# Kernel optimization log

Measured on AMD Instinct MI355X. Metric: run time of the kernel, lower is better.

## Reference

```python
import jax, jax.numpy as jnp
import numpy as np

NUM_HEADS = 8
NUM_CHUNKS, INPUT_DIM = 50000, 768
HIDDEN_DIM, OUTPUT_DIM = 512, 256
NUM_CELLS, MAX_LEN = 2048, 64


def setup_inputs() -> dict:
    key = jax.random.key(0)
    ks = jax.random.split(key, 16)
    s = 0.02
    return {
        "chunk_features": jax.random.normal(ks[0], (NUM_CHUNKS, INPUT_DIM), jnp.float32),
        # q/k/v input projections (nn.Linear: y = x @ W.T + b)
        "Wq": jax.random.normal(ks[1], (HIDDEN_DIM, INPUT_DIM), jnp.float32) * s,
        "bq": jnp.zeros((HIDDEN_DIM,), jnp.float32),
        "Wk": jax.random.normal(ks[2], (HIDDEN_DIM, INPUT_DIM), jnp.float32) * s,
        "bk": jnp.zeros((HIDDEN_DIM,), jnp.float32),
        "Wv": jax.random.normal(ks[3], (HIDDEN_DIM, INPUT_DIM), jnp.float32) * s,
        "bv": jnp.zeros((HIDDEN_DIM,), jnp.float32),
        # nn.MultiheadAttention internal in_proj (stacked q,k,v) and out_proj
        "W_in": jax.random.normal(ks[4], (3 * HIDDEN_DIM, HIDDEN_DIM), jnp.float32) * s,
        "b_in": jnp.zeros((3 * HIDDEN_DIM,), jnp.float32),
        "Wo": jax.random.normal(ks[5], (HIDDEN_DIM, HIDDEN_DIM), jnp.float32) * s,
        "bo": jnp.zeros((HIDDEN_DIM,), jnp.float32),
        # final output projection
        "Wout": jax.random.normal(ks[6], (OUTPUT_DIM, HIDDEN_DIM), jnp.float32) * s,
        "bout": jnp.zeros((OUTPUT_DIM,), jnp.float32),
        # ragged cells packed as padded indices + lengths
        "cell_idx": jax.random.randint(ks[7], (NUM_CELLS, MAX_LEN), 0, NUM_CHUNKS, jnp.int64),
        "cell_len": jax.random.randint(ks[8], (NUM_CELLS,), 0, MAX_LEN, jnp.int64),
    }


def reference(chunk_features, Wq, bq, Wk, bk, Wv, bv, W_in, b_in, Wo, bo,
              Wout, bout, cell_idx, cell_len):
    C, L = cell_idx.shape
    H = Wq.shape[0]
    hd = H // NUM_HEADS
    dt = chunk_features.dtype
    lengths = jnp.maximum(cell_len, 1)                       # at least 1 valid chunk per cell
    mask = jnp.arange(L)[None, :] < lengths[:, None]         # [C, L] valid-position mask

    x = chunk_features[cell_idx]                             # [C, L, D] ragged gather (padded)
    q = x @ Wq.T + bq                                        # [C, L, H]
    k = x @ Wk.T + bk
    v = x @ Wv.T + bv

    # MultiheadAttention's own in_proj on top of q/k/v
    Wiq, Wik, Wiv = jnp.split(W_in, 3, axis=0)
    biq, bik, biv = jnp.split(b_in, 3)
    qi = (q @ Wiq.T + biq).reshape(C, L, NUM_HEADS, hd)
    ki = (k @ Wik.T + bik).reshape(C, L, NUM_HEADS, hd)
    vi = (v @ Wiv.T + biv).reshape(C, L, NUM_HEADS, hd)

    scale = jnp.asarray(1.0 / np.sqrt(hd), dt)
    scores = jnp.einsum('clhd,cmhd->chlm', qi, ki) * scale   # [C, nH, L, L]
    scores = jnp.where(mask[:, None, None, :], scores, jnp.asarray(-1e30, dt))
    attn = jax.nn.softmax(scores, axis=-1)
    ctx = jnp.einsum('chlm,cmhd->clhd', attn, vi).reshape(C, L, H)
    out = ctx @ Wo.T + bo                                    # MHA out_proj

    # masked mean-pool over valid chunk positions, then final projection
    pooled = (out * mask[..., None]).sum(axis=1) / lengths[:, None].astype(dt)
    return pooled @ Wout.T + bout                            # [C, OUTPUT_DIM]
```

## Files before the change

kernel.cpp:

```cpp
#include <hip/hip_runtime.h>

typedef short s16x8 __attribute__((ext_vector_type(8)));
typedef float f32x4 __attribute__((ext_vector_type(4)));
typedef unsigned short u16;

static __device__ __forceinline__ f32x4 mfma16(s16x8 a, s16x8 b, f32x4 c) {
  return __builtin_amdgcn_mfma_f32_16x16x32_bf16(a, b, c, 0, 0, 0);
}

static __device__ __forceinline__ u16 f2b(float f) {
  union { float f; unsigned int u; } v; v.f = f;
  unsigned int u = v.u;
  return (u16)((u + 0x7fffu + ((u >> 16) & 1u)) >> 16);
}

static __device__ __forceinline__ void gld_lds16(const void* g, void* l) {
  __builtin_amdgcn_global_load_lds(
      (const __attribute__((address_space(1))) void*)g,
      (__attribute__((address_space(3))) void*)l, 16, 0, 0);
}

template<int MODE>
__global__ __launch_bounds__(256)
void gemm_pre(const float* __restrict__ A, const float* __restrict__ B,
              void* __restrict__ Cout, const float* __restrict__ bias,
              int M, int N, int K) {
  __shared__ u16 As[64][40];
  __shared__ u16 BsT[64][40];
  const int m0 = blockIdx.y << 6, n0 = blockIdx.x << 6;
  const int tid = threadIdx.x;
  const int wave = tid >> 6, lane = tid & 63;
  const int quad = lane >> 4, l16 = lane & 15;
  f32x4 acc[4] = {{0,0,0,0},{0,0,0,0},{0,0,0,0},{0,0,0,0}};
  for (int k0 = 0; k0 < K; k0 += 32) {
    __syncthreads();
    {
      const int r = tid >> 2, cs = (tid & 3) << 3;
      const float* ap = A + (size_t)(m0 + r) * K + k0 + cs;
      float4 v0 = *(const float4*)ap, v1 = *(const float4*)(ap + 4);
      As[r][cs+0] = f2b(v0.x); As[r][cs+1] = f2b(v0.y);
      As[r][cs+2] = f2b(v0.z); As[r][cs+3] = f2b(v0.w);
      As[r][cs+4] = f2b(v1.x); As[r][cs+5] = f2b(v1.y);
      As[r][cs+6] = f2b(v1.z); As[r][cs+7] = f2b(v1.w);
    }
    {
      const int kk = tid >> 3, ns = (tid & 7) << 3;
      const float* bp = B + (size_t)(k0 + kk) * N + n0 + ns;
      float4 v0 = *(const float4*)bp, v1 = *(const float4*)(bp + 4);
      BsT[ns+0][kk] = f2b(v0.x); BsT[ns+1][kk] = f2b(v0.y);
      BsT[ns+2][kk] = f2b(v0.z); BsT[ns+3][kk] = f2b(v0.w);
      BsT[ns+4][kk] = f2b(v1.x); BsT[ns+5][kk] = f2b(v1.y);
      BsT[ns+6][kk] = f2b(v1.z); BsT[ns+7][kk] = f2b(v1.w);
    }
    __syncthreads();
    const s16x8 af = *(const s16x8*)&As[(wave << 4) + l16][quad << 3];
    #pragma unroll
    for (int nt = 0; nt < 4; nt++) {
      const s16x8 bfr = *(const s16x8*)&BsT[(nt << 4) + l16][quad << 3];
      acc[nt] = mfma16(af, bfr, acc[nt]);
    }
  }
  const int mrow = m0 + (wave << 4) + (quad << 2);
  #pragma unroll
  for (int nt = 0; nt < 4; nt++) {
    const int n = n0 + (nt << 4) + l16;
    float badd = 0.f;
    if (MODE == 2) badd = bias[n];
    #pragma unroll
    for (int r = 0; r < 4; r++) {
      float v = acc[nt][r] + badd;
      if (MODE == 0)      ((u16*)Cout)[(size_t)(mrow + r) * N + n] = f2b(v);
      else if (MODE == 1) ((float*)Cout)[(size_t)n * M + (mrow + r)] = v;
      else                ((float*)Cout)[(size_t)(mrow + r) * N + n] = v;
    }
  }
}

__global__ __launch_bounds__(256)
void bias_dot(const float* __restrict__ A, const float* __restrict__ v,
              const float* __restrict__ c, float* __restrict__ out,
              int M, int K) {
  int j = blockIdx.x * 256 + threadIdx.x;
  if (j >= M) return;
  const float* ar = A + (size_t)j * K;
  float acc = 0.f;
  for (int k = 0; k < K; k += 4) {
    float4 w = *(const float4*)(ar + k);
    acc += w.x * v[k] + w.y * v[k+1] + w.z * v[k+2] + w.w * v[k+3];
  }
  out[j] = acc + c[j];
}

__global__ __launch_bounds__(256)
void convert_bf16(const float* __restrict__ src, u16* __restrict__ dst) {
  const size_t i = ((size_t)blockIdx.x * 256 + threadIdx.x) << 3;
  ushort4 lo, hi;
  if (i < (size_t)50000 * 768) {
    const float4 a = *(const float4*)(src + i);
    const float4 b = *(const float4*)(src + i + 4);
    lo.x = f2b(a.x); lo.y = f2b(a.y); lo.z = f2b(a.z); lo.w = f2b(a.w);
    hi.x = f2b(b.x); hi.y = f2b(b.y); hi.z = f2b(b.z); hi.w = f2b(b.w);
  } else {
    lo.x = lo.y = lo.z = lo.w = 0; hi.x = hi.y = hi.z = hi.w = 0;
  }
  *(ushort4*)(dst + i) = lo;
  *(ushort4*)(dst + i + 4) = hi;
}

__global__ __launch_bounds__(256)
void qkv_gemm(const u16* __restrict__ Xb, const u16* __restrict__ W,
              const float* __restrict__ bias, u16* __restrict__ QKV) {
  __shared__ u16 As[128 * 32];
  __shared__ u16 Bs[128 * 32];
  const int tid = threadIdx.x;
  const int wave = tid >> 6, lane = tid & 63;
  const int wm = wave >> 1, wn = wave & 1;
  const int quad = lane >> 4, l16 = lane & 15;
  const int m0 = blockIdx.y << 7, n0 = blockIdx.x << 7;

  const int r0 = (wave << 5) + (lane >> 2);
  const int cb = (lane & 3) << 3;
  const u16* gA = Xb + (size_t)(m0 + r0) * 768 + cb;
  const u16* gB = W  + (size_t)(n0 + r0) * 768 + cb;
  u16* lA = As + (wave << 10);
  u16* lB = Bs + (wave << 10);

  f32x4 acc[4][4];
  #pragma unroll
  for (int i = 0; i < 4; i++)
    #pragma unroll
    for (int j = 0; j < 4; j++) acc[i][j] = (f32x4){0.f, 0.f, 0.f, 0.f};

  for (int k0 = 0; k0 < 768; k0 += 32) {
    __syncthreads();
    gld_lds16(gA + k0,            lA);
    gld_lds16(gA + k0 + 16 * 768, lA + 512);
    gld_lds16(gB + k0,            lB);
    gld_lds16(gB + k0 + 16 * 768, lB + 512);
    __syncthreads();
    s16x8 af[4], bf[4];
    #pragma unroll
    for (int i = 0; i < 4; i++)
      af[i] = *(const s16x8*)(As + ((wm << 6) + (i << 4) + l16) * 32 + (quad << 3));
    #pragma unroll
    for (int j = 0; j < 4; j++)
      bf[j] = *(const s16x8*)(Bs + ((wn << 6) + (j << 4) + l16) * 32 + (quad << 3));
    #pragma unroll
    for (int i = 0; i < 4; i++)
      #pragma unroll
      for (int j = 0; j < 4; j++)
        acc[i][j] = mfma16(af[i], bf[j], acc[i][j]);
  }

  #pragma unroll
  for (int j = 0; j < 4; j++) {
    const int col = n0 + (wn << 6) + (j << 4) + l16;
    const float badd = bias[col];
    #pragma unroll
    for (int i = 0; i < 4; i++) {
      const int row = m0 + (wm << 6) + (i << 4) + (quad << 2);
      #pragma unroll
      for (int r = 0; r < 4; r++)
        QKV[(size_t)(row + r) * 1536 + col] = f2b(acc[i][j][r] + badd);
    }
  }
}

__global__ __launch_bounds__(256)
void attn2(const u16* __restrict__ QKV, const int* __restrict__ cell_idx,
           const int* __restrict__ cell_len, float* __restrict__ pooled_g) {
  __shared__ int idx_s[64];
  __shared__ u16 VT[64][72];
  __shared__ u16 Ps[64][72];
  __shared__ float Sf[64][66];
  __shared__ float pp[4][64];

  const int c = blockIdx.x, h = blockIdx.y;
  const int tid = threadIdx.x;
  const int wave = tid >> 6, lane = tid & 63;
  const int quad = lane >> 4, l16 = lane & 15;

  int len = cell_len[c];
  len = (len < 1) ? 1 : ((len > 64) ? 64 : len);
  const int mt = (len + 15) >> 4;
  const int Lr = mt << 4;
  const int kpv = (len + 31) >> 5;
  const float invLen = 1.0f / (float)len;

  if (tid < 64) idx_s[tid] = cell_idx[(c << 6) + tid];
  {
    const ushort4 z = {0, 0, 0, 0};
    u16* vz = &VT[0][0];
    u16* pz = &Ps[0][0];
    for (int i = tid; i < 1152; i += 256) {
      *(ushort4*)(vz + (i << 2)) = z;
      *(ushort4*)(pz + (i << 2)) = z;
    }
  }
  __syncthreads();

  for (int i = tid; i < (len << 3); i += 256) {
    const int r = i >> 3, seg = i & 7;
    const u16* src = QKV + (size_t)idx_s[r] * 1536 + 1024 + (h << 6) + (seg << 3);
    const ushort4 a = *(const ushort4*)src;
    const ushort4 b = *(const ushort4*)(src + 4);
    const int d0 = seg << 3;
    VT[d0+0][r] = a.x; VT[d0+1][r] = a.y; VT[d0+2][r] = a.z; VT[d0+3][r] = a.w;
    VT[d0+4][r] = b.x; VT[d0+5][r] = b.y; VT[d0+6][r] = b.z; VT[d0+7][r] = b.w;
  }

  for (int item = wave; item < mt * mt; item += 4) {
    const int mq = item / mt, mk = item - mq * mt;
    const size_t qrow = (size_t)idx_s[(mq << 4) + l16] * 1536;
    const size_t krow = (size_t)idx_s[(mk << 4) + l16] * 1536;
    f32x4 s = {0.f, 0.f, 0.f, 0.f};
    #pragma unroll
    for (int ks = 0; ks < 2; ks++) {
      const s16x8 a = *(const s16x8*)(QKV + qrow + (h << 6) + (ks << 5) + (quad << 3));
      const s16x8 b = *(const s16x8*)(QKV + krow + 512 + (h << 6) + (ks << 5) + (quad << 3));
      s = mfma16(a, b, s);
    }
    const int col = (mk << 4) + l16, rb = (mq << 4) + (quad << 2);
    Sf[rb+0][col] = s[0]; Sf[rb+1][col] = s[1];
    Sf[rb+2][col] = s[2]; Sf[rb+3][col] = s[3];
  }
  __syncthreads();

  {
    const int row = tid >> 2, sub = tid & 3, c0 = sub << 4;
    if (row < Lr) {
      float ev[16];
      float mx = -3e38f;
      #pragma unroll
      for (int t = 0; t < 16; t++) {
        const int cc = c0 + t;
        const float v = (cc < len) ? Sf[row][cc] : -3e38f;
        ev[t] = v; mx = fmaxf(mx, v);
      }
      mx = fmaxf(mx, __shfl_xor(mx, 1));
      mx = fmaxf(mx, __shfl_xor(mx, 2));
      float sum = 0.f;
      #pragma unroll
      for (int t = 0; t < 16; t++) {
        const int cc = c0 + t;
        const float e = (cc < len) ? __expf((ev[t] - mx) * 0.125f) : 0.f;
        ev[t] = e; sum += e;
      }
      sum += __shfl_xor(sum, 1);
      sum += __shfl_xor(sum, 2);
      const float inv = 1.0f / sum;
      #pragma unroll
      for (int t = 0; t < 16; t++) {
        const int cc = c0 + t;
        if (cc < len) Ps[row][cc] = f2b(ev[t] * inv);
      }
    }
  }
  __syncthreads();

  for (int item = wave; item < (mt << 2); item += 4) {
    const int mq = item >> 2, nd = item & 3;
    f32x4 s = {0.f, 0.f, 0.f, 0.f};
    for (int ks = 0; ks < kpv; ks++) {
      const s16x8 a = *(const s16x8*)&Ps[(mq << 4) + l16][(ks << 5) + (quad << 3)];
      const s16x8 b = *(const s16x8*)&VT[(nd << 4) + l16][(ks << 5) + (quad << 3)];
      s = mfma16(a, b, s);
    }
    const int col = (nd << 4) + l16, rb = (mq << 4) + (quad << 2);
    Sf[rb+0][col] = s[0]; Sf[rb+1][col] = s[1];
    Sf[rb+2][col] = s[2]; Sf[rb+3][col] = s[3];
  }
  __syncthreads();

  {
    float s = 0.f;
    for (int l = wave; l < len; l += 4) s += Sf[l][lane];
    pp[wave][lane] = s;
  }
  __syncthreads();
  if (tid < 64) {
    const float s = (pp[0][tid] + pp[1][tid] + pp[2][tid] + pp[3][tid]) * invLen;
    pooled_g[((size_t)c << 9) + (h << 6) + tid] = s;
  }
}

template<int MT>
static __device__ __forceinline__ void heads_loop(
    const u16* __restrict__ Wqkv, const float* __restrict__ b_eff,
    u16 (*Xs)[776], u16 (*Qs)[72], u16 (*Ks)[72], u16 (*VTs)[72],
    u16 (*Psf)[72], float (*Sf)[65], float* pooled,
    const int len, const float invLen, const int tid) {
  const int wave = tid >> 6, lane = tid & 63;
  const int quad = lane >> 4, l16 = lane & 15;
  constexpr int LR = MT * 16;
  constexpr int KPV = (LR + 31) / 32;
  const float scale = 0.125f;

  for (int h = 0; h < 8; h++) {
    f32x4 acc[3][MT];
    #pragma unroll
    for (int it = 0; it < 3; it++)
      #pragma unroll
      for (int im = 0; im < MT; im++) acc[it][im] = (f32x4){0.f,0.f,0.f,0.f};
    int grow[3], jcol[3];
    #pragma unroll
    for (int it = 0; it < 3; it++) {
      const int j = ((wave * 3 + it) << 4) + l16;
      const int sec = j >> 6;
      grow[it] = (sec << 9) + (h << 6) + (j & 63);
      jcol[it] = j;
    }
    s16x8 bcur[3];
    #pragma unroll
    for (int it = 0; it < 3; it++)
      bcur[it] = *(const s16x8*)(Wqkv + (size_t)grow[it] * 768 + (quad << 3));
    for (int ks = 0; ks < 24; ks++) {
      s16x8 bnext[3];
      const int ksn = (ks < 23) ? (ks + 1) : 23;
      #pragma unroll
      for (int it = 0; it < 3; it++)
        bnext[it] = *(const s16x8*)(Wqkv + (size_t)grow[it] * 768 + (ksn << 5) + (quad << 3));
      s16x8 af[MT];
      #pragma unroll
      for (int im = 0; im < MT; im++)
        af[im] = *(const s16x8*)&Xs[(im << 4) + l16][(ks << 5) + (quad << 3)];
      #pragma unroll
      for (int it = 0; it < 3; it++)
        #pragma unroll
        for (int im = 0; im < MT; im++)
          acc[it][im] = mfma16(af[im], bcur[it], acc[it][im]);
      bcur[0] = bnext[0]; bcur[1] = bnext[1]; bcur[2] = bnext[2];
    }
    #pragma unroll
    for (int it = 0; it < 3; it++) {
      const float badd = b_eff[grow[it]];
      const int j = jcol[it];
      #pragma unroll
      for (int im = 0; im < MT; im++) {
        const int rb = (im << 4) + (quad << 2);
        if (j < 64) {
          #pragma unroll
          for (int r = 0; r < 4; r++) Qs[rb + r][j] = f2b(acc[it][im][r] + badd);
        } else if (j < 128) {
          #pragma unroll
          for (int r = 0; r < 4; r++) Ks[rb + r][j - 64] = f2b(acc[it][im][r] + badd);
        } else {
          ushort4 hv;
          hv.x = f2b(acc[it][im][0] + badd);
          hv.y = f2b(acc[it][im][1] + badd);
          hv.z = f2b(acc[it][im][2] + badd);
          hv.w = f2b(acc[it][im][3] + badd);
          *(ushort4*)&VTs[j - 128][rb] = hv;
        }
      }
    }
    __syncthreads();
    for (int item = wave; item < MT * MT; item += 4) {
      const int mq = item / MT, mk = item - mq * MT;
      f32x4 sacc = (f32x4){0.f,0.f,0.f,0.f};
      #pragma unroll
      for (int ks = 0; ks < 2; ks++) {
        const s16x8 a = *(const s16x8*)&Qs[(mq << 4) + l16][(ks << 5) + (quad << 3)];
        const s16x8 b = *(const s16x8*)&Ks[(mk << 4) + l16][(ks << 5) + (quad << 3)];
        sacc = mfma16(a, b, sacc);
      }
      const int col = (mk << 4) + l16;
      const int rb = (mq << 4) + (quad << 2);
      #pragma unroll
      for (int r = 0; r < 4; r++) Sf[rb + r][col] = sacc[r];
    }
    __syncthreads();
    if (tid < LR) {
      float mx = -1e30f;
      for (int m = 0; m < len; m++) mx = fmaxf(mx, Sf[tid][m]);
      float sum = 0.f;
      for (int m = 0; m < len; m++) {
        const float e = __expf((Sf[tid][m] - mx) * scale);
        Sf[tid][m] = e;
        sum += e;
      }
      const float inv = 1.0f / sum;
      for (int m = 0; m < len; m++) Psf[tid][m] = f2b(Sf[tid][m] * inv);
    }
    __syncthreads();
    for (int item = wave; item < MT * 4; item += 4) {
      const int mq = item >> 2, nd = item & 3;
      f32x4 cacc = (f32x4){0.f,0.f,0.f,0.f};
      #pragma unroll
      for (int ks = 0; ks < KPV; ks++) {
        const s16x8 a = *(const s16x8*)&Psf[(mq << 4) + l16][(ks << 5) + (quad << 3)];
        const s16x8 b = *(const s16x8*)&VTs[(nd << 4) + l16][(ks << 5) + (quad << 3)];
        cacc = mfma16(a, b, cacc);
      }
      const int col = (nd << 4) + l16;
      const int rb = (mq << 4) + (quad << 2);
      #pragma unroll
      for (int r = 0; r < 4; r++) Sf[rb + r][col] = cacc[r];
    }
    __syncthreads();
    if (tid < 64) {
      float s = 0.f;
      for (int l = 0; l < len; l++) s += Sf[l][tid];
      pooled[(h << 6) + tid] = s * invLen;
    }
    __syncthreads();
  }
}

__global__ __launch_bounds__(256, 1)
void cell_attn(const float* __restrict__ chunk, const u16* __restrict__ Wqkv,
               const float* __restrict__ b_eff, const int* __restrict__ cell_idx,
               const int* __restrict__ cell_len, float* __restrict__ pooled_g) {
  __shared__ u16 Xs[64][776];
  __shared__ u16 Qs[64][72];
  __shared__ u16 Ks[64][72];
  __shared__ u16 VTs[64][72];
  __shared__ u16 Psf[64][72];
  __shared__ float Sf[64][65];
  __shared__ float pooled[512];
  __shared__ int idx_s[64];

  const int c = blockIdx.x;
  const int tid = threadIdx.x;

  int len = cell_len[c];
  len = (len < 1) ? 1 : ((len > 64) ? 64 : len);
  const int mt = (len + 15) >> 4;
  const int Lr = mt << 4;
  const float invLen = 1.0f / (float)len;

  if (tid < 64) idx_s[tid] = cell_idx[(c << 6) + tid];
  __syncthreads();

  for (int i = tid; i < len * 192; i += 256) {
    const int r = i / 192;
    const int c4 = i - r * 192;
    const float4 f = *(const float4*)(chunk + (size_t)idx_s[r] * 768 + (c4 << 2));
    ushort4 hv; hv.x = f2b(f.x); hv.y = f2b(f.y); hv.z = f2b(f.z); hv.w = f2b(f.w);
    *(ushort4*)&Xs[r][c4 << 2] = hv;
  }
  const ushort4 z4 = {0, 0, 0, 0};
  for (int i = tid; i < (Lr - len) * 192; i += 256) {
    const int r = len + i / 192;
    const int c4 = i - (i / 192) * 192;
    *(ushort4*)&Xs[r][c4 << 2] = z4;
  }
  for (int i = tid; i < 1152; i += 256) *(ushort4*)(&Psf[0][0] + (i << 2)) = z4;
  for (int i = tid; i < 1152; i += 256) *(ushort4*)(&VTs[0][0] + (i << 2)) = z4;
  __syncthreads();

  switch (mt) {
    case 1: heads_loop<1>(Wqkv, b_eff, Xs, Qs, Ks, VTs, Psf, Sf, pooled, len, invLen, tid); break;
    case 2: heads_loop<2>(Wqkv, b_eff, Xs, Qs, Ks, VTs, Psf, Sf, pooled, len, invLen, tid); break;
    case 3: heads_loop<3>(Wqkv, b_eff, Xs, Qs, Ks, VTs, Psf, Sf, pooled, len, invLen, tid); break;
    default: heads_loop<4>(Wqkv, b_eff, Xs, Qs, Ks, VTs, Psf, Sf, pooled, len, invLen, tid); break;
  }

  for (int i = tid; i < 512; i += 256) pooled_g[((size_t)c << 9) + i] = pooled[i];
}

extern "C" void kernel_launch(void* const* d_in, const int* in_sizes, int n_in,
                              void* d_out, int out_size, void* d_ws, size_t ws_size,
                              hipStream_t stream) {
  const float* chunk  = (const float*)d_in[0];
  const float* Wq     = (const float*)d_in[1];
  const float* bq     = (const float*)d_in[2];
  const float* Wk     = (const float*)d_in[3];
  const float* bk     = (const float*)d_in[4];
  const float* Wv     = (const float*)d_in[5];
  const float* bv     = (const float*)d_in[6];
  const float* W_in   = (const float*)d_in[7];
  const float* b_in   = (const float*)d_in[8];
  const float* Wo     = (const float*)d_in[9];
  const float* bo     = (const float*)d_in[10];
  const float* Wout   = (const float*)d_in[11];
  const float* bout   = (const float*)d_in[12];
  const int* cell_idx = (const int*)d_in[13];
  const int* cell_len = (const int*)d_in[14];

  char* ws = (char*)d_ws;
  u16*   Wqkv   = (u16*)(ws + 0);
  float* b_eff  = (float*)(ws + 2359296);
  float* WfT    = (float*)(ws + 2365440);
  float* bfe    = (float*)(ws + 2889728);
  float* pooled = (float*)(ws + 2890752);
  u16*   Xb     = (u16*)(ws + 7085056);
  u16*   QKV    = (u16*)(ws + 83958784);
  const size_t FAST_NEED = 237706240ull;
  const bool fast = (ws_size >= FAST_NEED);

  dim3 blk(256);
  dim3 g1(12, 8);
  gemm_pre<0><<<g1, blk, 0, stream>>>(W_in,            Wq, (void*)(Wqkv),            nullptr, 512, 768, 512);
  gemm_pre<0><<<g1, blk, 0, stream>>>(W_in + 512*512,  Wk, (void*)(Wqkv + 512*768),  nullptr, 512, 768, 512);
  gemm_pre<0><<<g1, blk, 0, stream>>>(W_in + 1024*512, Wv, (void*)(Wqkv + 1024*768), nullptr, 512, 768, 512);
  dim3 g2(8, 4);
  gemm_pre<1><<<g2, blk, 0, stream>>>(Wout, Wo, (void*)WfT, nullptr, 256, 512, 512);
  bias_dot<<<dim3(2), blk, 0, stream>>>(W_in,            bq, b_in,        b_eff,        512, 512);
  bias_dot<<<dim3(2), blk, 0, stream>>>(W_in + 512*512,  bk, b_in + 512,  b_eff + 512,  512, 512);
  bias_dot<<<dim3(2), blk, 0, stream>>>(W_in + 1024*512, bv, b_in + 1024, b_eff + 1024, 512, 512);
  bias_dot<<<dim3(1), blk, 0, stream>>>(Wout, bo, bout, bfe, 256, 512);

  if (fast) {
    convert_bf16<<<dim3(18768), blk, 0, stream>>>(chunk, Xb);
    qkv_gemm<<<dim3(12, 391), blk, 0, stream>>>(Xb, Wqkv, b_eff, QKV);
    attn2<<<dim3(2048, 8), blk, 0, stream>>>(QKV, cell_idx, cell_len, pooled);
  } else {
    cell_attn<<<dim3(2048), blk, 0, stream>>>(chunk, Wqkv, b_eff, cell_idx, cell_len, pooled);
  }

  dim3 g3(4, 32);
  gemm_pre<2><<<g3, blk, 0, stream>>>(pooled, WfT, d_out, bfe, 2048, 256, 512);
}
```

Before: 725.3 us.

## Skip per-chunk V projection by pooling attention weights over raw features

Mean pooling is linear, so the kernel now reduces each head's attention matrix to a single pooled weight vector. It applies those weights to the gathered raw bf16 chunk features and projects the result once through a precomposed per-head matrix (Wout·Wo·Wiv·Wv). This drops the V third of the large 50000-row projection GEMM, the V gather/transposition in the attention kernel, and the P·V MFMA. In exchange it adds a per-cell weighted gather of 768-wide feature rows, a K=6144 final GEMM, and extra weight-precomposition launches. The QK GEMM also gets an XCD-aware block swizzle.

```diff
diff --git a/kernel.cpp b/kernel.cpp
--- a/kernel.cpp
+++ b/kernel.cpp
@@ -13,6 +13,10 @@
   unsigned int u = v.u;
   return (u16)((u + 0x7fffu + ((u >> 16) & 1u)) >> 16);
 }
+static __device__ __forceinline__ float b2f(u16 h) {
+  union { float f; unsigned int u; } v; v.u = ((unsigned int)h) << 16;
+  return v.f;
+}
 
 static __device__ __forceinline__ void gld_lds16(const void* g, void* l) {
   __builtin_amdgcn_global_load_lds(
@@ -24,9 +28,12 @@
 __global__ __launch_bounds__(256)
 void gemm_pre(const float* __restrict__ A, const float* __restrict__ B,
               void* __restrict__ Cout, const float* __restrict__ bias,
-              int M, int N, int K) {
+              int M, int N, int K, int lda, int ldb, int ldc,
+              size_t za, size_t zb, size_t zc) {
   __shared__ u16 As[64][40];
   __shared__ u16 BsT[64][40];
+  A += za * blockIdx.z;  B += zb * blockIdx.z;
+  const size_t coff = zc * blockIdx.z;
   const int m0 = blockIdx.y << 6, n0 = blockIdx.x << 6;
   const int tid = threadIdx.x;
   const int wave = tid >> 6, lane = tid & 63;
@@ -36,7 +43,7 @@
     __syncthreads();
     {
       const int r = tid >> 2, cs = (tid & 3) << 3;
-      const float* ap = A + (size_t)(m0 + r) * K + k0 + cs;
+      const float* ap = A + (size_t)(m0 + r) * lda + k0 + cs;
       float4 v0 = *(const float4*)ap, v1 = *(const float4*)(ap + 4);
       As[r][cs+0] = f2b(v0.x); As[r][cs+1] = f2b(v0.y);
       As[r][cs+2] = f2b(v0.z); As[r][cs+3] = f2b(v0.w);
@@ -45,7 +52,7 @@
     }
     {
       const int kk = tid >> 3, ns = (tid & 7) << 3;
-      const float* bp = B + (size_t)(k0 + kk) * N + n0 + ns;
+      const float* bp = B + (size_t)(k0 + kk) * ldb + n0 + ns;
       float4 v0 = *(const float4*)bp, v1 = *(const float4*)(bp + 4);
       BsT[ns+0][kk] = f2b(v0.x); BsT[ns+1][kk] = f2b(v0.y);
       BsT[ns+2][kk] = f2b(v0.z); BsT[ns+3][kk] = f2b(v0.w);
@@ -69,9 +76,9 @@
     #pragma unroll
     for (int r = 0; r < 4; r++) {
       float v = acc[nt][r] + badd;
-      if (MODE == 0)      ((u16*)Cout)[(size_t)(mrow + r) * N + n] = f2b(v);
-      else if (MODE == 1) ((float*)Cout)[(size_t)n * M + (mrow + r)] = v;
-      else                ((float*)Cout)[(size_t)(mrow + r) * N + n] = v;
+      if (MODE == 0)      ((u16*)Cout)[coff + (size_t)(mrow + r) * ldc + n] = f2b(v);
+      else if (MODE == 1) ((float*)Cout)[coff + (size_t)n * ldc + (mrow + r)] = v;
+      else                ((float*)Cout)[coff + (size_t)(mrow + r) * ldc + n] = v;
     }
   }
 }
@@ -108,15 +115,19 @@
 }
 
 __global__ __launch_bounds__(256)
-void qkv_gemm(const u16* __restrict__ Xb, const u16* __restrict__ W,
-              const float* __restrict__ bias, u16* __restrict__ QKV) {
+void qk_gemm(const u16* __restrict__ Xb, const u16* __restrict__ W,
+             const float* __restrict__ bias, u16* __restrict__ QK2) {
   __shared__ u16 As[128 * 32];
   __shared__ u16 Bs[128 * 32];
+  const int g = blockIdx.x;
+  const int xcd = g & 7;
+  const int lin = xcd * 391 + (g >> 3);
+  const int n0 = (lin & 7) << 7;
+  const int m0 = (lin >> 3) << 7;
   const int tid = threadIdx.x;
   const int wave = tid >> 6, lane = tid & 63;
   const int wm = wave >> 1, wn = wave & 1;
   const int quad = lane >> 4, l16 = lane & 15;
-  const int m0 = blockIdx.y << 7, n0 = blockIdx.x << 7;
 
   const int r0 = (wave << 5) + (lane >> 2);
   const int cb = (lane & 3) << 3;
@@ -161,19 +172,16 @@
       const int row = m0 + (wm << 6) + (i << 4) + (quad << 2);
       #pragma unroll
       for (int r = 0; r < 4; r++)
-        QKV[(size_t)(row + r) * 1536 + col] = f2b(acc[i][j][r] + badd);
-    }
-  }
-}
-
-__global__ __launch_bounds__(256)
-void attn2(const u16* __restrict__ QKV, const int* __restrict__ cell_idx,
-           const int* __restrict__ cell_len, float* __restrict__ pooled_g) {
+        QK2[(size_t)(row + r) * 1024 + col] = f2b(acc[i][j][r] + badd);
+    }
+  }
+}
+
+__global__ __launch_bounds__(256)
+void attn2w(const u16* __restrict__ QK2, const int* __restrict__ cell_idx,
+            const int* __restrict__ cell_len, float* __restrict__ w_g) {
   __shared__ int idx_s[64];
-  __shared__ u16 VT[64][72];
-  __shared__ u16 Ps[64][72];
   __shared__ float Sf[64][66];
-  __shared__ float pp[4][64];
 
   const int c = blockIdx.x, h = blockIdx.y;
   const int tid = threadIdx.x;
@@ -183,41 +191,20 @@
   int len = cell_len[c];
   len = (len < 1) ? 1 : ((len > 64) ? 64 : len);
   const int mt = (len + 15) >> 4;
-  const int Lr = mt << 4;
-  const int kpv = (len + 31) >> 5;
   const float invLen = 1.0f / (float)len;
 
   if (tid < 64) idx_s[tid] = cell_idx[(c << 6) + tid];
-  {
-    const ushort4 z = {0, 0, 0, 0};
-    u16* vz = &VT[0][0];
-    u16* pz = &Ps[0][0];
-    for (int i = tid; i < 1152; i += 256) {
-      *(ushort4*)(vz + (i << 2)) = z;
-      *(ushort4*)(pz + (i << 2)) = z;
-    }
-  }
   __syncthreads();
-
-  for (int i = tid; i < (len << 3); i += 256) {
-    const int r = i >> 3, seg = i & 7;
-    const u16* src = QKV + (size_t)idx_s[r] * 1536 + 1024 + (h << 6) + (seg << 3);
-    const ushort4 a = *(const ushort4*)src;
-    const ushort4 b = *(const ushort4*)(src + 4);
-    const int d0 = seg << 3;
-    VT[d0+0][r] = a.x; VT[d0+1][r] = a.y; VT[d0+2][r] = a.z; VT[d0+3][r] = a.w;
-    VT[d0+4][r] = b.x; VT[d0+5][r] = b.y; VT[d0+6][r] = b.z; VT[d0+7][r] = b.w;
-  }
 
   for (int item = wave; item < mt * mt; item += 4) {
     const int mq = item / mt, mk = item - mq * mt;
-    const size_t qrow = (size_t)idx_s[(mq << 4) + l16] * 1536;
-    const size_t krow = (size_t)idx_s[(mk << 4) + l16] * 1536;
+    const size_t qrow = (size_t)idx_s[(mq << 4) + l16] * 1024;
+    const size_t krow = (size_t)idx_s[(mk << 4) + l16] * 1024;
     f32x4 s = {0.f, 0.f, 0.f, 0.f};
     #pragma unroll
     for (int ks = 0; ks < 2; ks++) {
-      const s16x8 a = *(const s16x8*)(QKV + qrow + (h << 6) + (ks << 5) + (quad << 3));
-      const s16x8 b = *(const s16x8*)(QKV + krow + 512 + (h << 6) + (ks << 5) + (quad << 3));
+      const s16x8 a = *(const s16x8*)(QK2 + qrow + (h << 6) + (ks << 5) + (quad << 3));
+      const s16x8 b = *(const s16x8*)(QK2 + krow + 512 + (h << 6) + (ks << 5) + (quad << 3));
       s = mfma16(a, b, s);
     }
     const int col = (mk << 4) + l16, rb = (mq << 4) + (quad << 2);
@@ -228,7 +215,7 @@
 
   {
     const int row = tid >> 2, sub = tid & 3, c0 = sub << 4;
-    if (row < Lr) {
+    if (row < len) {
       float ev[16];
       float mx = -3e38f;
       #pragma unroll
@@ -250,37 +237,100 @@
       sum += __shfl_xor(sum, 2);
       const float inv = 1.0f / sum;
       #pragma unroll
-      for (int t = 0; t < 16; t++) {
-        const int cc = c0 + t;
-        if (cc < len) Ps[row][cc] = f2b(ev[t] * inv);
-      }
+      for (int t = 0; t < 16; t++) Sf[row][c0 + t] = ev[t] * inv;
     }
   }
   __syncthreads();
 
-  for (int item = wave; item < (mt << 2); item += 4) {
-    const int mq = item >> 2, nd = item & 3;
-    f32x4 s = {0.f, 0.f, 0.f, 0.f};
-    for (int ks = 0; ks < kpv; ks++) {
-      const s16x8 a = *(const s16x8*)&Ps[(mq << 4) + l16][(ks << 5) + (quad << 3)];
-      const s16x8 b = *(const s16x8*)&VT[(nd << 4) + l16][(ks << 5) + (quad << 3)];
-      s = mfma16(a, b, s);
-    }
-    const int col = (nd << 4) + l16, rb = (mq << 4) + (quad << 2);
-    Sf[rb+0][col] = s[0]; Sf[rb+1][col] = s[1];
-    Sf[rb+2][col] = s[2]; Sf[rb+3][col] = s[3];
-  }
+  if (tid < 64) {
+    float s = 0.f;
+    if (tid < len)
+      for (int l = 0; l < len; l++) s += Sf[l][tid];
+    w_g[(size_t)((c << 3) + h) * 64 + tid] = s * invLen;
+  }
+}
+
+__global__ __launch_bounds__(256)
+void xbar_k(const u16* __restrict__ Xb, const float* __restrict__ w_g,
+            const int* __restrict__ cell_idx, const int* __restrict__ cell_len,
+            u16* __restrict__ Xbar) {
+  __shared__ int idx_s[64];
+  __shared__ float wl[512];
+  const int c = blockIdx.x;
+  const int tid = threadIdx.x;
+
+  int len = cell_len[c];
+  len = (len < 1) ? 1 : ((len > 64) ? 64 : len);
+
+  if (tid < 64) idx_s[tid] = cell_idx[(c << 6) + tid];
+  wl[tid] = w_g[((size_t)c << 9) + tid];
+  wl[tid + 256] = w_g[((size_t)c << 9) + tid + 256];
   __syncthreads();
 
-  {
-    float s = 0.f;
-    for (int l = wave; l < len; l += 4) s += Sf[l][lane];
-    pp[wave][lane] = s;
-  }
-  __syncthreads();
-  if (tid < 64) {
-    const float s = (pp[0][tid] + pp[1][tid] + pp[2][tid] + pp[3][tid]) * invLen;
-    pooled_g[((size_t)c << 9) + (h << 6) + tid] = s;
+  if (tid < 192) {
+    const int d0 = tid << 2;
+    float acc[8][4];
+    #pragma unroll
+    for (int h = 0; h < 8; h++)
+      #pragma unroll
+      for (int d = 0; d < 4; d++) acc[h][d] = 0.f;
+    for (int m = 0; m < len; m++) {
+      const ushort4 xv = *(const ushort4*)(Xb + (size_t)idx_s[m] * 768 + d0);
+      const float x0 = b2f(xv.x), x1 = b2f(xv.y), x2 = b2f(xv.z), x3 = b2f(xv.w);
+      #pragma unroll
+      for (int h = 0; h < 8; h++) {
+        const float wv = wl[(h << 6) + m];
+        acc[h][0] += wv * x0; acc[h][1] += wv * x1;
+        acc[h][2] += wv * x2; acc[h][3] += wv * x3;
+      }
+    }
+    #pragma unroll
+    for (int h = 0; h < 8; h++) {
+      ushort4 o;
+      o.x = f2b(acc[h][0]); o.y = f2b(acc[h][1]);
+      o.z = f2b(acc[h][2]); o.w = f2b(acc[h][3]);
+      *(ushort4*)(Xbar + (size_t)c * 6144 + (h * 768) + d0) = o;
+    }
+  }
+}
+
+__global__ __launch_bounds__(256)
+void gemm_final(const u16* __restrict__ A, const u16* __restrict__ B,
+                const float* __restrict__ bias, float* __restrict__ out) {
+  __shared__ u16 As[64 * 32];
+  __shared__ u16 Bs[64 * 32];
+  const int tid = threadIdx.x;
+  const int wave = tid >> 6, lane = tid & 63;
+  const int quad = lane >> 4, l16 = lane & 15;
+  const int m0 = blockIdx.y << 6, n0 = blockIdx.x << 6;
+
+  const int r = lane >> 2, c8 = (lane & 3) << 3;
+  const u16* gA = A + (size_t)(m0 + (wave << 4) + r) * 6144 + c8;
+  const u16* gB = B + (size_t)(n0 + (wave << 4) + r) * 6144 + c8;
+  u16* lA = As + (wave << 9);
+  u16* lB = Bs + (wave << 9);
+
+  f32x4 acc[4] = {{0,0,0,0},{0,0,0,0},{0,0,0,0},{0,0,0,0}};
+  for (int k0 = 0; k0 < 6144; k0 += 32) {
+    __syncthreads();
+    gld_lds16(gA + k0, lA);
+    gld_lds16(gB + k0, lB);
+    __syncthreads();
+    const s16x8 a = *(const s16x8*)(As + ((wave << 4) + l16) * 32 + (quad << 3));
+    #pragma unroll
+    for (int j = 0; j < 4; j++) {
+      const s16x8 b = *(const s16x8*)(Bs + ((j << 4) + l16) * 32 + (quad << 3));
+      acc[j] = mfma16(a, b, acc[j]);
+    }
+  }
+  const int row = m0 + (wave << 4) + (quad << 2);
+  #pragma unroll
+  for (int j = 0; j < 4; j++) {
+    const int col = n0 + (j << 4) + l16;
+    const float badd = bias[col];
+    #pragma unroll
+    for (int r2 = 0; r2 < 4; r2++)
+      out[(size_t)(row + r2) * 256 + col] = acc[j][r2] + badd;
   }
 }
 
@@ -484,31 +534,40 @@
   float* WfT    = (float*)(ws + 2365440);
   float* bfe    = (float*)(ws + 2889728);
   float* pooled = (float*)(ws + 2890752);
-  u16*   Xb     = (u16*)(ws + 7085056);
-  u16*   QKV    = (u16*)(ws + 83958784);
-  const size_t FAST_NEED = 237706240ull;
+  float* Wv_eff = (float*)(ws + 7085056);
+  float* Wf     = (float*)(ws + 8657920);
+  float* b2     = (float*)(ws + 9182208);
+  u16*   Mh     = (u16*)(ws + 9183232);
+  float* w_g    = (float*)(ws + 12328960);
+  u16*   Xbar   = (u16*)(ws + 16523264);
+  u16*   Xb     = (u16*)(ws + 41689088);
+  u16*   QK2    = (u16*)(ws + 118562816);
+  const size_t FAST_NEED = 221061120ull;
   const bool fast = (ws_size >= FAST_NEED);
 
   dim3 blk(256);
-  dim3 g1(12, 8);
-  gemm_pre<0><<<g1, blk, 0, stream>>>(W_in,            Wq, (void*)(Wqkv),            nullptr, 512, 768, 512);
-  gemm_pre<0><<<g1, blk, 0, stream>>>(W_in + 512*512,  Wk, (void*)(Wqkv + 512*768),  nullptr, 512, 768, 512);
-  gemm_pre<0><<<g1, blk, 0, stream>>>(W_in + 1024*512, Wv, (void*)(Wqkv + 1024*768), nullptr, 512, 768, 512);
-  dim3 g2(8, 4);
-  gemm_pre<1><<<g2, blk, 0, stream>>>(Wout, Wo, (void*)WfT, nullptr, 256, 512, 512);
+  gemm_pre<0><<<dim3(12, 8), blk, 0, stream>>>(W_in,           Wq, (void*)Wqkv,            nullptr, 512, 768, 512, 512, 768, 768, 0, 0, 0);
+  gemm_pre<0><<<dim3(12, 8), blk, 0, stream>>>(W_in + 512*512, Wk, (void*)(Wqkv + 512*768), nullptr, 512, 768, 512, 512, 768, 768, 0, 0, 0);
   bias_dot<<<dim3(2), blk, 0, stream>>>(W_in,            bq, b_in,        b_eff,        512, 512);
   bias_dot<<<dim3(2), blk, 0, stream>>>(W_in + 512*512,  bk, b_in + 512,  b_eff + 512,  512, 512);
   bias_dot<<<dim3(2), blk, 0, stream>>>(W_in + 1024*512, bv, b_in + 1024, b_eff + 1024, 512, 512);
   bias_dot<<<dim3(1), blk, 0, stream>>>(Wout, bo, bout, bfe, 256, 512);
 
   if (fast) {
+    gemm_pre<3><<<dim3(12, 8), blk, 0, stream>>>(W_in + 1024*512, Wv, (void*)Wv_eff, nullptr, 512, 768, 512, 512, 768, 768, 0, 0, 0);
+    gemm_pre<3><<<dim3(8, 4), blk, 0, stream>>>(Wout, Wo, (void*)Wf, nullptr, 256, 512, 512, 512, 512, 512, 0, 0, 0);
+    bias_dot<<<dim3(1), blk, 0, stream>>>(Wf, b_eff + 1024, bfe, b2, 256, 512);
+    gemm_pre<0><<<dim3(12, 4, 8), blk, 0, stream>>>(Wf, Wv_eff, (void*)Mh, nullptr,
+        256, 768, 64, 512, 768, 6144, (size_t)64, (size_t)64*768, (size_t)768);
     convert_bf16<<<dim3(18768), blk, 0, stream>>>(chunk, Xb);
-    qkv_gemm<<<dim3(12, 391), blk, 0, stream>>>(Xb, Wqkv, b_eff, QKV);
-    attn2<<<dim3(2048, 8), blk, 0, stream>>>(QKV, cell_idx, cell_len, pooled);
+    qk_gemm<<<dim3(3128), blk, 0, stream>>>(Xb, Wqkv, b_eff, QK2);
+    attn2w<<<dim3(2048, 8), blk, 0, stream>>>(QK2, cell_idx, cell_len, w_g);
+    xbar_k<<<dim3(2048), blk, 0, stream>>>(Xb, w_g, cell_idx, cell_len, Xbar);
+    gemm_final<<<dim3(4, 32), blk, 0, stream>>>(Xbar, Mh, b2, (float*)d_out);
   } else {
+    gemm_pre<0><<<dim3(12, 8), blk, 0, stream>>>(W_in + 1024*512, Wv, (void*)(Wqkv + 1024*768), nullptr, 512, 768, 512, 512, 768, 768, 0, 0, 0);
+    gemm_pre<1><<<dim3(8, 4), blk, 0, stream>>>(Wout, Wo, (void*)WfT, nullptr, 256, 512, 512, 512, 512, 256, 0, 0, 0);
     cell_attn<<<dim3(2048), blk, 0, stream>>>(chunk, Wqkv, b_eff, cell_idx, cell_len, pooled);
-  }
-
-  dim3 g3(4, 32);
-  gemm_pre<2><<<g3, blk, 0, stream>>>(pooled, WfT, d_out, bfe, 2048, 256, 512);
-}
+    gemm_pre<2><<<dim3(4, 32), blk, 0, stream>>>(pooled, WfT, d_out, bfe, 2048, 256, 512, 512, 256, 256, 0, 0, 0);
+  }
+}
```

Result: slower. 768.7 us (+6.0%).
